# Kernel optimization log

Hardware: AMD Instinct MI355X
Metric: run time of the kernel (lower is better)

## Reference

```python
import jax, jax.numpy as jnp
import numpy as np

N_NODES = 100000
N_EDGES = 3200000
D_IN, D_HID, D_OUT = 128, 128, 40


def _sage_conv(x, src, dst, W_l, W_r, b, counts):
    # mean aggregation of neighbor (source) features at destination nodes
    agg = jax.ops.segment_sum(x[src], dst, num_segments=N_NODES)  # [N, d]
    agg = agg / counts  # mean (isolated nodes stay zero via clamped counts)
    # PyG SAGEConv: out = lin_l(aggr) + lin_r(x_root); bias lives in lin_l
    return agg @ W_l + x @ W_r + b


def setup_inputs() -> dict:
    key = jax.random.key(0)
    ks = jax.random.split(key, 8)
    x = jax.random.normal(ks[0], (N_NODES, D_IN), dtype=jnp.float32)
    edge_index = jax.random.randint(ks[1], (2, N_EDGES), 0, N_NODES, dtype=jnp.int64)
    s1 = 1.0 / np.sqrt(D_IN)
    s2 = 1.0 / np.sqrt(D_HID)
    return {
        "x": x,
        "edge_index": edge_index,
        "W1_l": jax.random.uniform(ks[2], (D_IN, D_HID), jnp.float32, -s1, s1),
        "W1_r": jax.random.uniform(ks[3], (D_IN, D_HID), jnp.float32, -s1, s1),
        "b1": jnp.zeros((D_HID,), jnp.float32),
        "W2_l": jax.random.uniform(ks[4], (D_HID, D_OUT), jnp.float32, -s2, s2),
        "W2_r": jax.random.uniform(ks[5], (D_HID, D_OUT), jnp.float32, -s2, s2),
        "b2": jnp.zeros((D_OUT,), jnp.float32),
    }


def reference(x, edge_index, W1_l, W1_r, b1, W2_l, W2_r, b2):
    src, dst = edge_index[0], edge_index[1]
    # in-degree per destination node, clamped to avoid div-by-zero
    deg = jax.ops.segment_sum(jnp.ones((N_EDGES,), jnp.float32), dst, num_segments=N_NODES)
    counts = jnp.maximum(deg, 1.0)[:, None]  # [N, 1]
    h = jax.nn.relu(_sage_conv(x, src, dst, W1_l, W1_r, b1, counts))
    h = _sage_conv(h, src, dst, W2_l, W2_r, b2, counts)
    return jax.nn.log_softmax(h, axis=1)
```

## Files before the change

kernel.cpp:

```cpp
#include <hip/hip_runtime.h>
#include <hip/hip_bf16.h>
#include <hip/hip_fp8.h>
#include <math.h>

#define N_NODES 100000
#define D_IN    128
#define D_HID   128
#define D_OUT   40
#define NBUCK   391
#define CHUNK   4096
#define SLABCAP 16320


using short8  = __attribute__((ext_vector_type(8))) short;
using float4v = __attribute__((ext_vector_type(4))) float;
using floatx2 = __attribute__((ext_vector_type(2))) float;

__device__ __forceinline__ unsigned short f2b(float f) {
    __hip_bfloat16 b = __float2bfloat16(f);
    return *(unsigned short*)&b;
}
__device__ __forceinline__ unsigned packb(float a, float b) {
    return (unsigned)f2b(a) | ((unsigned)f2b(b) << 16);
}

__device__ __forceinline__ unsigned char f2q(float f) {
    __hip_fp8_e4m3 v(f);
    return *(unsigned char*)&v;
}
template <int SEL>
__device__ __forceinline__ float q2f(unsigned u) {
#if __has_builtin(__builtin_amdgcn_cvt_f32_fp8)
    return __builtin_amdgcn_cvt_f32_fp8((int)u, SEL);
#else
    unsigned char b = (u >> (SEL * 8)) & 0xff;
    __hip_fp8_e4m3 v;
    *(unsigned char*)&v = b;
    return (float)v;
#endif
}
template <bool HI>
__device__ __forceinline__ floatx2 pkcvt(unsigned u) {
#if __has_builtin(__builtin_amdgcn_cvt_pk_f32_fp8)
    return __builtin_amdgcn_cvt_pk_f32_fp8((int)u, HI);
#else
    floatx2 r;
    if constexpr (HI) { r[0] = q2f<2>(u); r[1] = q2f<3>(u); }
    else              { r[0] = q2f<0>(u); r[1] = q2f<1>(u); }
    return r;
#endif
}

__global__ void detect_kernel(const int* __restrict__ ei, int* __restrict__ flag) {
    if (threadIdx.x == 0 && blockIdx.x == 0) {
        int all0 = 1;
        for (int i = 0; i < 256; ++i) {
            if (ei[2 * i + 1] != 0) { all0 = 0; break; }
        }
        *flag = all0;
    }
}

__device__ __forceinline__ long long edge_at(const void* ei, int is64, long long idx) {
    if (is64) return ((const long long*)ei)[idx];
    return (long long)((const int*)ei)[idx];
}

__global__ __launch_bounds__(256) void cast_kernel(const float* __restrict__ x,
                                                   unsigned short* __restrict__ xb,
                                                   unsigned char* __restrict__ xq) {
    long long i = ((long long)blockIdx.x * 256 + threadIdx.x) * 8;
    if (i >= (long long)N_NODES * 128) return;
    float4 a = *(const float4*)&x[i];
    float4 b = *(const float4*)&x[i + 4];
    ushort4 o0, o1;
    o0.x = f2b(a.x); o0.y = f2b(a.y); o0.z = f2b(a.z); o0.w = f2b(a.w);
    o1.x = f2b(b.x); o1.y = f2b(b.y); o1.z = f2b(b.z); o1.w = f2b(b.w);
    *(ushort4*)&xb[i] = o0;
    *(ushort4*)&xb[i + 4] = o1;
    uint2 p;
    p.x = (unsigned)f2q(a.x) | ((unsigned)f2q(a.y) << 8)
        | ((unsigned)f2q(a.z) << 16) | ((unsigned)f2q(a.w) << 24);
    p.y = (unsigned)f2q(b.x) | ((unsigned)f2q(b.y) << 8)
        | ((unsigned)f2q(b.z) << 16) | ((unsigned)f2q(b.w) << 24);
    *(uint2*)&xq[i] = p;
}

__global__ __launch_bounds__(256) void pack_w_kernel(const float* __restrict__ W1l,
                                                     const float* __restrict__ W1r,
                                                     const float* __restrict__ W2l,
                                                     const float* __restrict__ W2r,
                                                     unsigned short* __restrict__ wp1,
                                                     unsigned short* __restrict__ wp2) {
    int t = blockIdx.x * 256 + threadIdx.x;
    if (t < 4096) {
        int lane = t & 63;
        int ks = (t >> 6) & 7;
        int ct = t >> 9;
        int n = ct * 16 + (lane & 15);
        int kr = (lane >> 4) * 8;
        unsigned short v[8];
#pragma unroll
        for (int j = 0; j < 8; ++j) {
            int k = ks * 32 + kr + j;
            float f = (k < 128) ? W1l[k * 128 + n] : W1r[(k - 128) * 128 + n];
            v[j] = f2b(f);
        }
        ushort4 o0 = {v[0], v[1], v[2], v[3]};
        ushort4 o1 = {v[4], v[5], v[6], v[7]};
        *(ushort4*)&wp1[t * 8] = o0;
        *(ushort4*)&wp1[t * 8 + 4] = o1;
    } else if (t < 4096 + 1280) {
        int u = t - 4096;
        int lane = u & 63;
        int ks = (u >> 6) & 3;
        int ct = u >> 8;
        int n = ct * 16 + (lane & 15);
        int kr = (lane >> 4) * 8;
        unsigned short v[8];
#pragma unroll
        for (int j = 0; j < 8; ++j) {
            int k = ks * 32 + kr + j;
            float f = (n < 40) ? W2l[k * 40 + n] : W2r[k * 40 + (n - 40)];
            v[j] = f2b(f);
        }
        ushort4 o0 = {v[0], v[1], v[2], v[3]};
        ushort4 o1 = {v[4], v[5], v[6], v[7]};
        *(ushort4*)&wp2[u * 8] = o0;
        *(ushort4*)&wp2[u * 8 + 4] = o1;
    }
}

__global__ __launch_bounds__(1024) void partition_kernel(const void* __restrict__ ei,
                                                         const int* __restrict__ flag,
                                                         unsigned* __restrict__ bcount,
                                                         unsigned* __restrict__ slab,
                                                         long long E) {
    __shared__ unsigned hist[NBUCK];
    __shared__ unsigned lstart[NBUCK];
    __shared__ unsigned gofs[NBUCK];
    __shared__ unsigned s[512];
    __shared__ unsigned rec[CHUNK];
    __shared__ unsigned short bkt[CHUNK];

    const int tid = threadIdx.x;
    const int is64 = *flag;
    const long long cb = (long long)blockIdx.x * CHUNK;
    const unsigned n = (unsigned)(((E - cb) < (long long)CHUNK) ? (E - cb) : CHUNK);

    if (tid < NBUCK) hist[tid] = 0;
    __syncthreads();

#pragma unroll
    for (int j = 0; j < CHUNK / 1024; ++j) {
        unsigned e = j * 1024 + tid;
        if (e < n) {
            unsigned d = (unsigned)edge_at(ei, is64, E + cb + e);
            atomicAdd(&hist[d >> 8], 1u);
        }
    }
    __syncthreads();

    if (tid < 512) s[tid] = (tid < NBUCK) ? hist[tid] : 0u;
    __syncthreads();
    for (int off = 1; off < 512; off <<= 1) {
        unsigned t = 0;
        if (tid < 512 && tid >= off) t = s[tid - off];
        __syncthreads();
        if (tid < 512) s[tid] += t;
        __syncthreads();
    }
    if (tid < NBUCK) {
        unsigned cnt = hist[tid];
        unsigned ex = s[tid] - cnt;
        lstart[tid] = ex;
        if (cnt) {
            unsigned g = atomicAdd(&bcount[tid], cnt);
            gofs[tid] = (unsigned)(tid * SLABCAP) + g - ex;
        }
        hist[tid] = 0;
    }
    __syncthreads();

#pragma unroll
    for (int j = 0; j < CHUNK / 1024; ++j) {
        unsigned e = j * 1024 + tid;
        if (e < n) {
            unsigned sv = (unsigned)edge_at(ei, is64, cb + e);
            unsigned d  = (unsigned)edge_at(ei, is64, E + cb + e);
            unsigned b = d >> 8;
            unsigned loc = atomicAdd(&hist[b], 1u);
            unsigned slot = lstart[b] + loc;
            rec[slot] = ((d & 255u) << 17) | sv;
            bkt[slot] = (unsigned short)b;
        }
    }
    __syncthreads();

#pragma unroll
    for (int j = 0; j < CHUNK / 1024; ++j) {
        unsigned i = j * 1024 + tid;
        if (i < n) {
            unsigned b = bkt[i];
            slab[gofs[b] + i] = rec[i];
        }
    }
}

__global__ __launch_bounds__(512) void bscan_kernel(const unsigned* __restrict__ bcount,
                                                    unsigned* __restrict__ bstart) {
    __shared__ unsigned s[512];
    int tid = threadIdx.x;
    unsigned v = (tid < NBUCK) ? bcount[tid] : 0u;
    s[tid] = v;
    __syncthreads();
    for (int off = 1; off < 512; off <<= 1) {
        unsigned t = (tid >= off) ? s[tid - off] : 0u;
        __syncthreads();
        s[tid] += t;
        __syncthreads();
    }
    if (tid < NBUCK) bstart[tid] = s[tid] - v;
    if (tid == 511) bstart[NBUCK] = s[511];
}

__global__ __launch_bounds__(256) void build_kernel(const unsigned* __restrict__ slab,
                                                    const unsigned* __restrict__ bstart,
                                                    unsigned* __restrict__ deg,
                                                    float* __restrict__ invc,
                                                    unsigned* __restrict__ row_start,
                                                    int* __restrict__ csr) {
    __shared__ unsigned cnt[256];
    __shared__ unsigned scn[256];
    const int tid = threadIdx.x;
    const int nb = blockIdx.x << 8;
    const unsigned es = bstart[blockIdx.x];
    const unsigned n  = bstart[blockIdx.x + 1] - es;
    const long long sb = (long long)blockIdx.x * SLABCAP;

    cnt[tid] = 0;
    __syncthreads();
    for (unsigned i = tid; i < n; i += 256) {
        unsigned d = slab[sb + i] >> 17;
        atomicAdd(&cnt[d], 1u);
    }
    __syncthreads();
    unsigned v = cnt[tid];
    scn[tid] = v;
    __syncthreads();
    for (int off = 1; off < 256; off <<= 1) {
        unsigned t = (tid >= off) ? scn[tid - off] : 0u;
        __syncthreads();
        scn[tid] += t;
        __syncthreads();
    }
    unsigned ex = scn[tid] - v;
    int node = nb + tid;
    if (node < N_NODES) {
        deg[node] = v;
        invc[node] = 1.0f / fmaxf((float)v, 1.0f);
        row_start[node] = es + ex;
    }
    __syncthreads();
    cnt[tid] = ex;
    __syncthreads();
    for (unsigned i = tid; i < n; i += 256) {
        unsigned pr = slab[sb + i];
        unsigned d = pr >> 17;
        unsigned pos = es + atomicAdd(&cnt[d], 1u);
        csr[pos] = (int)(pr & 0x1FFFFu);
    }
}

__global__ __launch_bounds__(256) void gather_fp8_kernel(const unsigned char* __restrict__ featq,
                                                         const int* __restrict__ csr,
                                                         const unsigned* __restrict__ row_start,
                                                         const unsigned* __restrict__ deg,
                                                         const float* __restrict__ invc,
                                                         unsigned short* __restrict__ aggb) {
    const int wave = threadIdx.x >> 6;
    const int lane = threadIdx.x & 63;
    const int node = blockIdx.x * 4 + wave;
    if (node >= N_NODES) return;

    const unsigned start = row_start[node];
    const unsigned cnt = deg[node];
    const int s = lane >> 4;
    const int cg = lane & 15;

    floatx2 acc[4];
#pragma unroll
    for (int k = 0; k < 4; ++k) acc[k] = (floatx2){0.f, 0.f};

    for (unsigned base = 0; base < cnt; base += 64) {
        unsigned rem = cnt - base;
        if (rem > 64u) rem = 64u;
        int nid = (lane < (int)rem) ? csr[start + base + lane] : 0;
        for (unsigned j = 0; j < rem; j += 8) {
            uint2 u0 = {0u, 0u}, u1 = {0u, 0u};
            unsigned i0 = j + s;
            unsigned i1 = j + 4 + s;
            int s0 = __shfl(nid, (int)(i0 & 63));
            int s1 = __shfl(nid, (int)(i1 & 63));
            if (i0 < rem) u0 = *(const uint2*)&featq[(long long)s0 * 128 + cg * 8];
            if (i1 < rem) u1 = *(const uint2*)&featq[(long long)s1 * 128 + cg * 8];
            acc[0] += pkcvt<false>(u0.x); acc[1] += pkcvt<true>(u0.x);
            acc[2] += pkcvt<false>(u0.y); acc[3] += pkcvt<true>(u0.y);
            acc[0] += pkcvt<false>(u1.x); acc[1] += pkcvt<true>(u1.x);
            acc[2] += pkcvt<false>(u1.y); acc[3] += pkcvt<true>(u1.y);
        }
    }

#pragma unroll
    for (int k = 0; k < 4; ++k) {
        acc[k][0] += __shfl_xor(acc[k][0], 16);
        acc[k][1] += __shfl_xor(acc[k][1], 16);
        acc[k][0] += __shfl_xor(acc[k][0], 32);
        acc[k][1] += __shfl_xor(acc[k][1], 32);
    }

    if (lane < 16) {
        const float ic = invc[node];
        uint4 o;
        o.x = packb(acc[0][0] * ic, acc[0][1] * ic);
        o.y = packb(acc[1][0] * ic, acc[1][1] * ic);
        o.z = packb(acc[2][0] * ic, acc[2][1] * ic);
        o.w = packb(acc[3][0] * ic, acc[3][1] * ic);
        *(uint4*)&aggb[(long long)node * 128 + cg * 8] = o;
    }
}

__global__ __launch_bounds__(256) void gemm1_mfma_kernel(const unsigned short* __restrict__ aggb,
                                                         const unsigned short* __restrict__ xb,
                                                         const unsigned short* __restrict__ wp1,
                                                         const float* __restrict__ bias,
                                                         unsigned short* __restrict__ hb) {
    const int wave = threadIdx.x >> 6;
    const int lane = threadIdx.x & 63;
    const int row0 = blockIdx.x * 64 + wave * 16;
    const long long abase = (long long)(row0 + (lane & 15)) * 128 + (lane >> 4) * 8;

    float4v acc[8];
#pragma unroll
    for (int ct = 0; ct < 8; ++ct) acc[ct] = (float4v){0.f, 0.f, 0.f, 0.f};

#pragma unroll
    for (int ks = 0; ks < 8; ++ks) {
        union { uint4 u; short8 s; } af;
        if (ks < 4) af.u = *(const uint4*)&aggb[abase + ks * 32];
        else        af.u = *(const uint4*)&xb[abase + (ks - 4) * 32];
#pragma unroll
        for (int ct = 0; ct < 8; ++ct) {
            union { uint4 u; short8 s; } bf;
            bf.u = *(const uint4*)&wp1[((ct * 8 + ks) * 64 + lane) * 8];
            acc[ct] = __builtin_amdgcn_mfma_f32_16x16x32_bf16(af.s, bf.s, acc[ct], 0, 0, 0);
        }
    }

    const int crow0 = row0 + (lane >> 4) * 4;
    const int ccol = lane & 15;
#pragma unroll
    for (int ct = 0; ct < 8; ++ct) {
        const int col = ct * 16 + ccol;
        const float bv = bias[col];
#pragma unroll
        for (int r = 0; r < 4; ++r) {
            int row = crow0 + r;
            if (row < N_NODES)
                hb[(long long)row * 128 + col] = f2b(fmaxf(acc[ct][r] + bv, 0.0f));
        }
    }
}

__global__ __launch_bounds__(256) void gemm2p_mfma_kernel(const unsigned short* __restrict__ hb,
                                                          const unsigned short* __restrict__ wp2,
                                                          const float* __restrict__ b2,
                                                          unsigned char* __restrict__ pq,
                                                          float* __restrict__ q) {
    const int wave = threadIdx.x >> 6;
    const int lane = threadIdx.x & 63;
    const int row0 = blockIdx.x * 64 + wave * 16;
    const long long abase = (long long)(row0 + (lane & 15)) * 128 + (lane >> 4) * 8;

    float4v acc[5];
#pragma unroll
    for (int ct = 0; ct < 5; ++ct) acc[ct] = (float4v){0.f, 0.f, 0.f, 0.f};

#pragma unroll
    for (int ks = 0; ks < 4; ++ks) {
        union { uint4 u; short8 s; } af;
        af.u = *(const uint4*)&hb[abase + ks * 32];
#pragma unroll
        for (int ct = 0; ct < 5; ++ct) {
            union { uint4 u; short8 s; } bf;
            bf.u = *(const uint4*)&wp2[((ct * 4 + ks) * 64 + lane) * 8];
            acc[ct] = __builtin_amdgcn_mfma_f32_16x16x32_bf16(af.s, bf.s, acc[ct], 0, 0, 0);
        }
    }

    const int crow0 = row0 + (lane >> 4) * 4;
    const int ccol = lane & 15;
#pragma unroll
    for (int ct = 0; ct < 5; ++ct) {
        const int col = ct * 16 + ccol;
#pragma unroll
        for (int r = 0; r < 4; ++r) {
            int row = crow0 + r;
            if (row < N_NODES) {
                if (col < D_OUT) {
                    pq[(long long)row * D_OUT + col] = f2q(acc[ct][r]);
                } else {
                    q[(long long)row * D_OUT + (col - D_OUT)] = acc[ct][r] + b2[col - D_OUT];
                }
            }
        }
    }
}

__global__ __launch_bounds__(256) void gather40_kernel(const unsigned char* __restrict__ pq,
                                                       const float* __restrict__ q,
                                                       const int* __restrict__ csr,
                                                       const unsigned* __restrict__ row_start,
                                                       const unsigned* __restrict__ deg,
                                                       const float* __restrict__ invc,
                                                       float* __restrict__ out) {
    __shared__ float sm[4][40];
    const int wave = threadIdx.x >> 6;
    const int lane = threadIdx.x & 63;
    const int node = blockIdx.x * 4 + wave;
    if (node >= N_NODES) return;

    const unsigned start = row_start[node];
    const unsigned cnt = deg[node];
    const int s = lane / 10;
    const int cg = lane % 10;
    const bool gactive = s < 6;

    floatx2 a01 = (floatx2){0.f, 0.f}, a23 = (floatx2){0.f, 0.f};

    for (unsigned base = 0; base < cnt; base += 64) {
        unsigned rem = cnt - base;
        if (rem > 64u) rem = 64u;
        int nid = (lane < (int)rem) ? csr[start + base + lane] : 0;
        for (unsigned j = 0; j < rem; j += 24) {
            unsigned u[4];
#pragma unroll
            for (int t = 0; t < 4; ++t) {
                unsigned idx = j + t * 6 + s;
                int sid = __shfl(nid, (int)(idx & 63));
                bool valid = gactive && (idx < rem);
                u[t] = valid ? *(const unsigned*)&pq[(long long)sid * D_OUT + cg * 4] : 0u;
            }
#pragma unroll
            for (int t = 0; t < 4; ++t) {
                a01 += pkcvt<false>(u[t]);
                a23 += pkcvt<true>(u[t]);
            }
        }
    }

    float a0 = a01[0], a1 = a01[1], a2 = a23[0], a3 = a23[1];
    {
        float t0, t1, t2, t3;
        t0 = __shfl(a0, lane + 30); t1 = __shfl(a1, lane + 30);
        t2 = __shfl(a2, lane + 30); t3 = __shfl(a3, lane + 30);
        if (lane < 30) { a0 += t0; a1 += t1; a2 += t2; a3 += t3; }
        t0 = __shfl(a0, lane + 20); t1 = __shfl(a1, lane + 20);
        t2 = __shfl(a2, lane + 20); t3 = __shfl(a3, lane + 20);
        if (lane < 10) { a0 += t0; a1 += t1; a2 += t2; a3 += t3; }
        t0 = __shfl(a0, lane + 10); t1 = __shfl(a1, lane + 10);
        t2 = __shfl(a2, lane + 10); t3 = __shfl(a3, lane + 10);
        if (lane < 10) { a0 += t0; a1 += t1; a2 += t2; a3 += t3; }
    }
    if (lane < 10) {
        sm[wave][cg * 4 + 0] = a0;
        sm[wave][cg * 4 + 1] = a1;
        sm[wave][cg * 4 + 2] = a2;
        sm[wave][cg * 4 + 3] = a3;
    }
    const bool active = lane < D_OUT;
    float v = active ? (sm[wave][active ? lane : 0] * invc[node]
                        + q[(long long)node * D_OUT + (active ? lane : 0)])
                     : -__builtin_huge_valf();
    float m = v;
#pragma unroll
    for (int off = 32; off >= 1; off >>= 1) m = fmaxf(m, __shfl_xor(m, off));
    float e = active ? expf(v - m) : 0.0f;
    float ssum = e;
#pragma unroll
    for (int off = 32; off >= 1; off >>= 1) ssum += __shfl_xor(ssum, off);
    float ls = logf(ssum);
    if (active) out[(long long)node * D_OUT + lane] = v - m - ls;
}

extern "C" void kernel_launch(void* const* d_in, const int* in_sizes, int n_in,
                              void* d_out, int out_size, void* d_ws, size_t ws_size,
                              hipStream_t stream) {
    const float* x   = (const float*)d_in[0];
    const void*  ei  = d_in[1];
    const float* W1l = (const float*)d_in[2];
    const float* W1r = (const float*)d_in[3];
    const float* b1  = (const float*)d_in[4];
    const float* W2l = (const float*)d_in[5];
    const float* W2r = (const float*)d_in[6];
    const float* b2  = (const float*)d_in[7];
    float* out = (float*)d_out;

    const long long E = (long long)in_sizes[1] / 2;
    const int NPB = (int)((E + CHUNK - 1) / CHUNK);

    char* ws = (char*)d_ws;
    int*      flag      = (int*)ws;
    unsigned* bcount    = (unsigned*)(ws + 4096);
    unsigned* bstart    = (unsigned*)(ws + 8192);
    unsigned* deg       = (unsigned*)(ws + 16384);
    float*    invc      = (float*)(ws + 416384);
    unsigned* row_start = (unsigned*)(ws + 816384);
    int*      csr       = (int*)(ws + 1216384);
    unsigned short* xb  = (unsigned short*)(ws + 14016384);
    unsigned char*  pq  = (unsigned char*)(ws + 14016384);
    float*    q         = (float*)(ws + 22016384);
    unsigned short* aggb= (unsigned short*)(ws + 39616384);
    unsigned* slab      = (unsigned*)(ws + 39616384);
    unsigned short* wp1 = (unsigned short*)(ws + 65216384);
    unsigned short* wp2 = (unsigned short*)(ws + 65281920);
    unsigned short* hb  = (unsigned short*)(ws + 65310720);
    unsigned char*  xq  = (unsigned char*)(ws + 90910720);

    (void)hipMemsetAsync(bcount, 0, 4096, stream);
    detect_kernel<<<1, 64, 0, stream>>>((const int*)ei, flag);

    cast_kernel<<<(int)(((long long)N_NODES * 128 / 8 + 255) / 256), 256, 0, stream>>>(x, xb, xq);
    pack_w_kernel<<<21, 256, 0, stream>>>(W1l, W1r, W2l, W2r, wp1, wp2);

    partition_kernel<<<NPB, 1024, 0, stream>>>(ei, flag, bcount, slab, E);
    bscan_kernel<<<1, 512, 0, stream>>>(bcount, bstart);
    build_kernel<<<NBUCK, 256, 0, stream>>>(slab, bstart, deg, invc, row_start, csr);

    gather_fp8_kernel<<<(N_NODES + 3) / 4, 256, 0, stream>>>(xq, csr, row_start, deg, invc, aggb);
    gemm1_mfma_kernel<<<(N_NODES + 63) / 64, 256, 0, stream>>>(aggb, xb, wp1, b1, hb);

    gemm2p_mfma_kernel<<<(N_NODES + 63) / 64, 256, 0, stream>>>(hb, wp2, b2, pq, q);
    gather40_kernel<<<(N_NODES + 3) / 4, 256, 0, stream>>>(pq, q, csr, row_start, deg, invc, out);
}
```

Measured before the change: 356.6 us.

## Split FP8 feature gather into four column-slice passes for cache locality

The FP8 node features are stored as four column slices of 32 bytes per node instead of one 128-byte row per node. The layer-1 gather then runs as four passes, each gathering a single slice for all nodes. Each slice is about 3.2 MB, so it can stay resident in L2/MALL during its pass and cut DRAM traffic from random neighbour reads. The cost is reading the CSR, degrees and row starts four times, extra launches, and smaller 32-byte random accesses per neighbour.

```diff
diff --git a/kernel.cpp b/kernel.cpp
--- a/kernel.cpp
+++ b/kernel.cpp
@@ -10,6 +10,7 @@
 #define NBUCK   391
 #define CHUNK   4096
 #define SLABCAP 16320
+#define SLICE_BYTES (N_NODES * 32)
 
 
 using short8  = __attribute__((ext_vector_type(8))) short;
@@ -68,9 +69,11 @@
 
 __global__ __launch_bounds__(256) void cast_kernel(const float* __restrict__ x,
                                                    unsigned short* __restrict__ xb,
-                                                   unsigned char* __restrict__ xq) {
+                                                   unsigned char* __restrict__ xq4) {
     long long i = ((long long)blockIdx.x * 256 + threadIdx.x) * 8;
     if (i >= (long long)N_NODES * 128) return;
+    long long node = i >> 7;
+    int col = (int)(i & 127);
     float4 a = *(const float4*)&x[i];
     float4 b = *(const float4*)&x[i + 4];
     ushort4 o0, o1;
@@ -83,7 +86,7 @@
         | ((unsigned)f2q(a.z) << 16) | ((unsigned)f2q(a.w) << 24);
     p.y = (unsigned)f2q(b.x) | ((unsigned)f2q(b.y) << 8)
         | ((unsigned)f2q(b.z) << 16) | ((unsigned)f2q(b.w) << 24);
-    *(uint2*)&xq[i] = p;
+    *(uint2*)&xq4[(long long)(col >> 5) * SLICE_BYTES + node * 32 + (col & 31)] = p;
 }
 
 __global__ __launch_bounds__(256) void pack_w_kernel(const float* __restrict__ W1l,
@@ -272,12 +275,13 @@
     }
 }
 
-__global__ __launch_bounds__(256) void gather_fp8_kernel(const unsigned char* __restrict__ featq,
-                                                         const int* __restrict__ csr,
-                                                         const unsigned* __restrict__ row_start,
-                                                         const unsigned* __restrict__ deg,
-                                                         const float* __restrict__ invc,
-                                                         unsigned short* __restrict__ aggb) {
+__global__ __launch_bounds__(256) void gather_fp8_pass_kernel(const unsigned char* __restrict__ slice,
+                                                              const int* __restrict__ csr,
+                                                              const unsigned* __restrict__ row_start,
+                                                              const unsigned* __restrict__ deg,
+                                                              const float* __restrict__ invc,
+                                                              unsigned short* __restrict__ aggb,
+                                                              int pass) {
     const int wave = threadIdx.x >> 6;
     const int lane = threadIdx.x & 63;
     const int node = blockIdx.x * 4 + wave;
@@ -285,8 +289,8 @@
 
     const unsigned start = row_start[node];
     const unsigned cnt = deg[node];
-    const int s = lane >> 4;
-    const int cg = lane & 15;
+    const int s = lane >> 2;
+    const int cg = lane & 3;
 
     floatx2 acc[4];
 #pragma unroll
@@ -296,14 +300,14 @@
         unsigned rem = cnt - base;
         if (rem > 64u) rem = 64u;
         int nid = (lane < (int)rem) ? csr[start + base + lane] : 0;
-        for (unsigned j = 0; j < rem; j += 8) {
+        for (unsigned j = 0; j < rem; j += 32) {
             uint2 u0 = {0u, 0u}, u1 = {0u, 0u};
-            unsigned i0 = j + s;
-            unsigned i1 = j + 4 + s;
+            unsigned i0 = j + (unsigned)s;
+            unsigned i1 = j + 16 + (unsigned)s;
             int s0 = __shfl(nid, (int)(i0 & 63));
             int s1 = __shfl(nid, (int)(i1 & 63));
-            if (i0 < rem) u0 = *(const uint2*)&featq[(long long)s0 * 128 + cg * 8];
-            if (i1 < rem) u1 = *(const uint2*)&featq[(long long)s1 * 128 + cg * 8];
+            if (i0 < rem) u0 = *(const uint2*)&slice[(long long)s0 * 32 + cg * 8];
+            if (i1 < rem) u1 = *(const uint2*)&slice[(long long)s1 * 32 + cg * 8];
             acc[0] += pkcvt<false>(u0.x); acc[1] += pkcvt<true>(u0.x);
             acc[2] += pkcvt<false>(u0.y); acc[3] += pkcvt<true>(u0.y);
             acc[0] += pkcvt<false>(u1.x); acc[1] += pkcvt<true>(u1.x);
@@ -313,20 +317,24 @@
 
 #pragma unroll
     for (int k = 0; k < 4; ++k) {
+        acc[k][0] += __shfl_xor(acc[k][0], 4);
+        acc[k][1] += __shfl_xor(acc[k][1], 4);
+        acc[k][0] += __shfl_xor(acc[k][0], 8);
+        acc[k][1] += __shfl_xor(acc[k][1], 8);
         acc[k][0] += __shfl_xor(acc[k][0], 16);
         acc[k][1] += __shfl_xor(acc[k][1], 16);
         acc[k][0] += __shfl_xor(acc[k][0], 32);
         acc[k][1] += __shfl_xor(acc[k][1], 32);
     }
 
-    if (lane < 16) {
+    if (lane < 4) {
         const float ic = invc[node];
         uint4 o;
         o.x = packb(acc[0][0] * ic, acc[0][1] * ic);
         o.y = packb(acc[1][0] * ic, acc[1][1] * ic);
         o.z = packb(acc[2][0] * ic, acc[2][1] * ic);
         o.w = packb(acc[3][0] * ic, acc[3][1] * ic);
-        *(uint4*)&aggb[(long long)node * 128 + cg * 8] = o;
+        *(uint4*)&aggb[(long long)node * 128 + pass * 32 + cg * 8] = o;
     }
 }
 
@@ -525,19 +533,22 @@
     unsigned short* wp1 = (unsigned short*)(ws + 65216384);
     unsigned short* wp2 = (unsigned short*)(ws + 65281920);
     unsigned short* hb  = (unsigned short*)(ws + 65310720);
-    unsigned char*  xq  = (unsigned char*)(ws + 90910720);
+    unsigned char*  xq4 = (unsigned char*)(ws + 90910720);
 
     (void)hipMemsetAsync(bcount, 0, 4096, stream);
     detect_kernel<<<1, 64, 0, stream>>>((const int*)ei, flag);
 
-    cast_kernel<<<(int)(((long long)N_NODES * 128 / 8 + 255) / 256), 256, 0, stream>>>(x, xb, xq);
+    cast_kernel<<<(int)(((long long)N_NODES * 128 / 8 + 255) / 256), 256, 0, stream>>>(x, xb, xq4);
     pack_w_kernel<<<21, 256, 0, stream>>>(W1l, W1r, W2l, W2r, wp1, wp2);
 
     partition_kernel<<<NPB, 1024, 0, stream>>>(ei, flag, bcount, slab, E);
     bscan_kernel<<<1, 512, 0, stream>>>(bcount, bstart);
     build_kernel<<<NBUCK, 256, 0, stream>>>(slab, bstart, deg, invc, row_start, csr);
 
-    gather_fp8_kernel<<<(N_NODES + 3) / 4, 256, 0, stream>>>(xq, csr, row_start, deg, invc, aggb);
+    for (int p = 0; p < 4; ++p) {
+        gather_fp8_pass_kernel<<<(N_NODES + 3) / 4, 256, 0, stream>>>(
+            xq4 + (long long)p * SLICE_BYTES, csr, row_start, deg, invc, aggb, p);
+    }
     gemm1_mfma_kernel<<<(N_NODES + 63) / 64, 256, 0, stream>>>(aggb, xb, wp1, b1, hb);
 
     gemm2p_mfma_kernel<<<(N_NODES + 63) / 64, 256, 0, stream>>>(hb, wp2, b2, pq, q);
```

Measured after the change: 466.3 us. 30.8% more time.

## Fuse neighbor gather into GEMM1 via shared memory and merge prep kernels

Applied to the files above, without the earlier changes.

Combines the fp8 neighbor-mean gather and the first SAGE GEMM into one kernel, staging each block's 64 aggregated rows in LDS instead of writing and rereading a bf16 aggregate buffer in global memory. Also merges the edge-format detection, feature cast and weight packing into a single launch. This removes a full intermediate round trip and two launches. In exchange, each wave now processes 16 nodes sequentially before the MFMA stage, reducing the number of independent waves available to hide gather latency.

```diff
diff --git a/kernel.cpp b/kernel.cpp
--- a/kernel.cpp
+++ b/kernel.cpp
@@ -10,6 +10,7 @@
 #define NBUCK   391
 #define CHUNK   4096
 #define SLABCAP 16320
+#define CAST_BLOCKS 6250
 
 
 using short8  = __attribute__((ext_vector_type(8))) short;
@@ -51,83 +52,85 @@
 #endif
 }
 
-__global__ void detect_kernel(const int* __restrict__ ei, int* __restrict__ flag) {
-    if (threadIdx.x == 0 && blockIdx.x == 0) {
-        int all0 = 1;
-        for (int i = 0; i < 256; ++i) {
-            if (ei[2 * i + 1] != 0) { all0 = 0; break; }
-        }
-        *flag = all0;
-    }
-}
-
 __device__ __forceinline__ long long edge_at(const void* ei, int is64, long long idx) {
     if (is64) return ((const long long*)ei)[idx];
     return (long long)((const int*)ei)[idx];
 }
 
-__global__ __launch_bounds__(256) void cast_kernel(const float* __restrict__ x,
+__global__ __launch_bounds__(256) void prep_kernel(const float* __restrict__ x,
                                                    unsigned short* __restrict__ xb,
-                                                   unsigned char* __restrict__ xq) {
-    long long i = ((long long)blockIdx.x * 256 + threadIdx.x) * 8;
-    if (i >= (long long)N_NODES * 128) return;
-    float4 a = *(const float4*)&x[i];
-    float4 b = *(const float4*)&x[i + 4];
-    ushort4 o0, o1;
-    o0.x = f2b(a.x); o0.y = f2b(a.y); o0.z = f2b(a.z); o0.w = f2b(a.w);
-    o1.x = f2b(b.x); o1.y = f2b(b.y); o1.z = f2b(b.z); o1.w = f2b(b.w);
-    *(ushort4*)&xb[i] = o0;
-    *(ushort4*)&xb[i + 4] = o1;
-    uint2 p;
-    p.x = (unsigned)f2q(a.x) | ((unsigned)f2q(a.y) << 8)
-        | ((unsigned)f2q(a.z) << 16) | ((unsigned)f2q(a.w) << 24);
-    p.y = (unsigned)f2q(b.x) | ((unsigned)f2q(b.y) << 8)
-        | ((unsigned)f2q(b.z) << 16) | ((unsigned)f2q(b.w) << 24);
-    *(uint2*)&xq[i] = p;
-}
-
-__global__ __launch_bounds__(256) void pack_w_kernel(const float* __restrict__ W1l,
-                                                     const float* __restrict__ W1r,
-                                                     const float* __restrict__ W2l,
-                                                     const float* __restrict__ W2r,
-                                                     unsigned short* __restrict__ wp1,
-                                                     unsigned short* __restrict__ wp2) {
-    int t = blockIdx.x * 256 + threadIdx.x;
-    if (t < 4096) {
-        int lane = t & 63;
-        int ks = (t >> 6) & 7;
-        int ct = t >> 9;
-        int n = ct * 16 + (lane & 15);
-        int kr = (lane >> 4) * 8;
-        unsigned short v[8];
-#pragma unroll
-        for (int j = 0; j < 8; ++j) {
-            int k = ks * 32 + kr + j;
-            float f = (k < 128) ? W1l[k * 128 + n] : W1r[(k - 128) * 128 + n];
-            v[j] = f2b(f);
-        }
-        ushort4 o0 = {v[0], v[1], v[2], v[3]};
-        ushort4 o1 = {v[4], v[5], v[6], v[7]};
-        *(ushort4*)&wp1[t * 8] = o0;
-        *(ushort4*)&wp1[t * 8 + 4] = o1;
-    } else if (t < 4096 + 1280) {
-        int u = t - 4096;
-        int lane = u & 63;
-        int ks = (u >> 6) & 3;
-        int ct = u >> 8;
-        int n = ct * 16 + (lane & 15);
-        int kr = (lane >> 4) * 8;
-        unsigned short v[8];
-#pragma unroll
-        for (int j = 0; j < 8; ++j) {
-            int k = ks * 32 + kr + j;
-            float f = (n < 40) ? W2l[k * 40 + n] : W2r[k * 40 + (n - 40)];
-            v[j] = f2b(f);
-        }
-        ushort4 o0 = {v[0], v[1], v[2], v[3]};
-        ushort4 o1 = {v[4], v[5], v[6], v[7]};
-        *(ushort4*)&wp2[u * 8] = o0;
-        *(ushort4*)&wp2[u * 8 + 4] = o1;
+                                                   unsigned char* __restrict__ xq,
+                                                   const float* __restrict__ W1l,
+                                                   const float* __restrict__ W1r,
+                                                   const float* __restrict__ W2l,
+                                                   const float* __restrict__ W2r,
+                                                   unsigned short* __restrict__ wp1,
+                                                   unsigned short* __restrict__ wp2,
+                                                   const int* __restrict__ ei,
+                                                   int* __restrict__ flag) {
+    const int b = blockIdx.x;
+    if (b < CAST_BLOCKS) {
+        long long i = ((long long)b * 256 + threadIdx.x) * 8;
+        if (i >= (long long)N_NODES * 128) return;
+        float4 a = *(const float4*)&x[i];
+        float4 c = *(const float4*)&x[i + 4];
+        ushort4 o0, o1;
+        o0.x = f2b(a.x); o0.y = f2b(a.y); o0.z = f2b(a.z); o0.w = f2b(a.w);
+        o1.x = f2b(c.x); o1.y = f2b(c.y); o1.z = f2b(c.z); o1.w = f2b(c.w);
+        *(ushort4*)&xb[i] = o0;
+        *(ushort4*)&xb[i + 4] = o1;
+        uint2 p;
+        p.x = (unsigned)f2q(a.x) | ((unsigned)f2q(a.y) << 8)
+            | ((unsigned)f2q(a.z) << 16) | ((unsigned)f2q(a.w) << 24);
+        p.y = (unsigned)f2q(c.x) | ((unsigned)f2q(c.y) << 8)
+            | ((unsigned)f2q(c.z) << 16) | ((unsigned)f2q(c.w) << 24);
+        *(uint2*)&xq[i] = p;
+    } else if (b < CAST_BLOCKS + 21) {
+        int t = (b - CAST_BLOCKS) * 256 + threadIdx.x;
+        if (t < 4096) {
+            int lane = t & 63;
+            int ks = (t >> 6) & 7;
+            int ct = t >> 9;
+            int n = ct * 16 + (lane & 15);
+            int kr = (lane >> 4) * 8;
+            unsigned short v[8];
+#pragma unroll
+            for (int j = 0; j < 8; ++j) {
+                int k = ks * 32 + kr + j;
+                float f = (k < 128) ? W1l[k * 128 + n] : W1r[(k - 128) * 128 + n];
+                v[j] = f2b(f);
+            }
+            ushort4 o0 = {v[0], v[1], v[2], v[3]};
+            ushort4 o1 = {v[4], v[5], v[6], v[7]};
+            *(ushort4*)&wp1[t * 8] = o0;
+            *(ushort4*)&wp1[t * 8 + 4] = o1;
+        } else if (t < 4096 + 1280) {
+            int u = t - 4096;
+            int lane = u & 63;
+            int ks = (u >> 6) & 3;
+            int ct = u >> 8;
+            int n = ct * 16 + (lane & 15);
+            int kr = (lane >> 4) * 8;
+            unsigned short v[8];
+#pragma unroll
+            for (int j = 0; j < 8; ++j) {
+                int k = ks * 32 + kr + j;
+                float f = (n < 40) ? W2l[k * 40 + n] : W2r[k * 40 + (n - 40)];
+                v[j] = f2b(f);
+            }
+            ushort4 o0 = {v[0], v[1], v[2], v[3]};
+            ushort4 o1 = {v[4], v[5], v[6], v[7]};
+            *(ushort4*)&wp2[u * 8] = o0;
+            *(ushort4*)&wp2[u * 8 + 4] = o1;
+        }
+    } else {
+        if (threadIdx.x == 0) {
+            int all0 = 1;
+            for (int i = 0; i < 256; ++i) {
+                if (ei[2 * i + 1] != 0) { all0 = 0; break; }
+            }
+            *flag = all0;
+        }
     }
 }
 
@@ -272,88 +275,92 @@
     }
 }
 
-__global__ __launch_bounds__(256) void gather_fp8_kernel(const unsigned char* __restrict__ featq,
-                                                         const int* __restrict__ csr,
-                                                         const unsigned* __restrict__ row_start,
-                                                         const unsigned* __restrict__ deg,
-                                                         const float* __restrict__ invc,
-                                                         unsigned short* __restrict__ aggb) {
+__global__ __launch_bounds__(256) void gather_gemm1_kernel(const unsigned char* __restrict__ featq,
+                                                           const int* __restrict__ csr,
+                                                           const unsigned* __restrict__ row_start,
+                                                           const unsigned* __restrict__ deg,
+                                                           const float* __restrict__ invc,
+                                                           const unsigned short* __restrict__ xb,
+                                                           const unsigned short* __restrict__ wp1,
+                                                           const float* __restrict__ bias,
+                                                           unsigned short* __restrict__ hb) {
+    __shared__ unsigned short sagg[64][136];
     const int wave = threadIdx.x >> 6;
     const int lane = threadIdx.x & 63;
-    const int node = blockIdx.x * 4 + wave;
-    if (node >= N_NODES) return;
-
-    const unsigned start = row_start[node];
-    const unsigned cnt = deg[node];
+    const int nblk = blockIdx.x * 64;
     const int s = lane >> 4;
     const int cg = lane & 15;
 
-    floatx2 acc[4];
-#pragma unroll
-    for (int k = 0; k < 4; ++k) acc[k] = (floatx2){0.f, 0.f};
-
-    for (unsigned base = 0; base < cnt; base += 64) {
-        unsigned rem = cnt - base;
-        if (rem > 64u) rem = 64u;
-        int nid = (lane < (int)rem) ? csr[start + base + lane] : 0;
-        for (unsigned j = 0; j < rem; j += 8) {
-            uint2 u0 = {0u, 0u}, u1 = {0u, 0u};
-            unsigned i0 = j + s;
-            unsigned i1 = j + 4 + s;
-            int s0 = __shfl(nid, (int)(i0 & 63));
-            int s1 = __shfl(nid, (int)(i1 & 63));
-            if (i0 < rem) u0 = *(const uint2*)&featq[(long long)s0 * 128 + cg * 8];
-            if (i1 < rem) u1 = *(const uint2*)&featq[(long long)s1 * 128 + cg * 8];
-            acc[0] += pkcvt<false>(u0.x); acc[1] += pkcvt<true>(u0.x);
-            acc[2] += pkcvt<false>(u0.y); acc[3] += pkcvt<true>(u0.y);
-            acc[0] += pkcvt<false>(u1.x); acc[1] += pkcvt<true>(u1.x);
-            acc[2] += pkcvt<false>(u1.y); acc[3] += pkcvt<true>(u1.y);
-        }
-    }
-
-#pragma unroll
-    for (int k = 0; k < 4; ++k) {
-        acc[k][0] += __shfl_xor(acc[k][0], 16);
-        acc[k][1] += __shfl_xor(acc[k][1], 16);
-        acc[k][0] += __shfl_xor(acc[k][0], 32);
-        acc[k][1] += __shfl_xor(acc[k][1], 32);
-    }
-
-    if (lane < 16) {
-        const float ic = invc[node];
-        uint4 o;
-        o.x = packb(acc[0][0] * ic, acc[0][1] * ic);
-        o.y = packb(acc[1][0] * ic, acc[1][1] * ic);
-        o.z = packb(acc[2][0] * ic, acc[2][1] * ic);
-        o.w = packb(acc[3][0] * ic, acc[3][1] * ic);
-        *(uint4*)&aggb[(long long)node * 128 + cg * 8] = o;
-    }
-}
-
-__global__ __launch_bounds__(256) void gemm1_mfma_kernel(const unsigned short* __restrict__ aggb,
-                                                         const unsigned short* __restrict__ xb,
-                                                         const unsigned short* __restrict__ wp1,
-                                                         const float* __restrict__ bias,
-                                                         unsigned short* __restrict__ hb) {
-    const int wave = threadIdx.x >> 6;
-    const int lane = threadIdx.x & 63;
-    const int row0 = blockIdx.x * 64 + wave * 16;
-    const long long abase = (long long)(row0 + (lane & 15)) * 128 + (lane >> 4) * 8;
-
-    float4v acc[8];
-#pragma unroll
-    for (int ct = 0; ct < 8; ++ct) acc[ct] = (float4v){0.f, 0.f, 0.f, 0.f};
+    for (int i = 0; i < 16; ++i) {
+        const int node = nblk + wave * 16 + i;
+        if (node < N_NODES) {
+            const unsigned start = row_start[node];
+            const unsigned cnt = deg[node];
+            floatx2 acc[4];
+#pragma unroll
+            for (int k = 0; k < 4; ++k) acc[k] = (floatx2){0.f, 0.f};
+
+            for (unsigned base = 0; base < cnt; base += 64) {
+                unsigned rem = cnt - base;
+                if (rem > 64u) rem = 64u;
+                int nid = (lane < (int)rem) ? csr[start + base + lane] : 0;
+                for (unsigned j = 0; j < rem; j += 8) {
+                    uint2 u0 = {0u, 0u}, u1 = {0u, 0u};
+                    unsigned i0 = j + s;
+                    unsigned i1 = j + 4 + s;
+                    int s0 = __shfl(nid, (int)(i0 & 63));
+                    int s1 = __shfl(nid, (int)(i1 & 63));
+                    if (i0 < rem) u0 = *(const uint2*)&featq[(long long)s0 * 128 + cg * 8];
+                    if (i1 < rem) u1 = *(const uint2*)&featq[(long long)s1 * 128 + cg * 8];
+                    acc[0] += pkcvt<false>(u0.x); acc[1] += pkcvt<true>(u0.x);
+                    acc[2] += pkcvt<false>(u0.y); acc[3] += pkcvt<true>(u0.y);
+                    acc[0] += pkcvt<false>(u1.x); acc[1] += pkcvt<true>(u1.x);
+                    acc[2] += pkcvt<false>(u1.y); acc[3] += pkcvt<true>(u1.y);
+                }
+            }
+
+#pragma unroll
+            for (int k = 0; k < 4; ++k) {
+                acc[k][0] += __shfl_xor(acc[k][0], 16);
+                acc[k][1] += __shfl_xor(acc[k][1], 16);
+                acc[k][0] += __shfl_xor(acc[k][0], 32);
+                acc[k][1] += __shfl_xor(acc[k][1], 32);
+            }
+
+            if (lane < 16) {
+                const float ic = invc[node];
+                uint4 o;
+                o.x = packb(acc[0][0] * ic, acc[0][1] * ic);
+                o.y = packb(acc[1][0] * ic, acc[1][1] * ic);
+                o.z = packb(acc[2][0] * ic, acc[2][1] * ic);
+                o.w = packb(acc[3][0] * ic, acc[3][1] * ic);
+                *(uint4*)&sagg[wave * 16 + i][cg * 8] = o;
+            }
+        } else if (lane < 16) {
+            uint4 z = {0u, 0u, 0u, 0u};
+            *(uint4*)&sagg[wave * 16 + i][cg * 8] = z;
+        }
+    }
+    __syncthreads();
+
+    const int row0 = nblk + wave * 16;
+    const unsigned short* aptr = &sagg[wave * 16 + (lane & 15)][(lane >> 4) * 8];
+    const long long xbase = (long long)(row0 + (lane & 15)) * 128 + (lane >> 4) * 8;
+
+    float4v gacc[8];
+#pragma unroll
+    for (int ct = 0; ct < 8; ++ct) gacc[ct] = (float4v){0.f, 0.f, 0.f, 0.f};
 
 #pragma unroll
     for (int ks = 0; ks < 8; ++ks) {
         union { uint4 u; short8 s; } af;
-        if (ks < 4) af.u = *(const uint4*)&aggb[abase + ks * 32];
-        else        af.u = *(const uint4*)&xb[abase + (ks - 4) * 32];
+        if (ks < 4) af.u = *(const uint4*)&aptr[ks * 32];
+        else        af.u = *(const uint4*)&xb[xbase + (ks - 4) * 32];
 #pragma unroll
         for (int ct = 0; ct < 8; ++ct) {
             union { uint4 u; short8 s; } bf;
             bf.u = *(const uint4*)&wp1[((ct * 8 + ks) * 64 + lane) * 8];
-            acc[ct] = __builtin_amdgcn_mfma_f32_16x16x32_bf16(af.s, bf.s, acc[ct], 0, 0, 0);
+            gacc[ct] = __builtin_amdgcn_mfma_f32_16x16x32_bf16(af.s, bf.s, gacc[ct], 0, 0, 0);
         }
     }
 
@@ -367,7 +374,7 @@
         for (int r = 0; r < 4; ++r) {
             int row = crow0 + r;
             if (row < N_NODES)
-                hb[(long long)row * 128 + col] = f2b(fmaxf(acc[ct][r] + bv, 0.0f));
+                hb[(long long)row * 128 + col] = f2b(fmaxf(gacc[ct][r] + bv, 0.0f));
         }
     }
 }
@@ -520,7 +527,6 @@
     unsigned short* xb  = (unsigned short*)(ws + 14016384);
     unsigned char*  pq  = (unsigned char*)(ws + 14016384);
     float*    q         = (float*)(ws + 22016384);
-    unsigned short* aggb= (unsigned short*)(ws + 39616384);
     unsigned* slab      = (unsigned*)(ws + 39616384);
     unsigned short* wp1 = (unsigned short*)(ws + 65216384);
     unsigned short* wp2 = (unsigned short*)(ws + 65281920);
@@ -528,17 +534,16 @@
     unsigned char*  xq  = (unsigned char*)(ws + 90910720);
 
     (void)hipMemsetAsync(bcount, 0, 4096, stream);
-    detect_kernel<<<1, 64, 0, stream>>>((const int*)ei, flag);
-
-    cast_kernel<<<(int)(((long long)N_NODES * 128 / 8 + 255) / 256), 256, 0, stream>>>(x, xb, xq);
-    pack_w_kernel<<<21, 256, 0, stream>>>(W1l, W1r, W2l, W2r, wp1, wp2);
+
+    prep_kernel<<<CAST_BLOCKS + 21 + 1, 256, 0, stream>>>(x, xb, xq, W1l, W1r, W2l, W2r,
+                                                          wp1, wp2, (const int*)ei, flag);
 
     partition_kernel<<<NPB, 1024, 0, stream>>>(ei, flag, bcount, slab, E);
     bscan_kernel<<<1, 512, 0, stream>>>(bcount, bstart);
     build_kernel<<<NBUCK, 256, 0, stream>>>(slab, bstart, deg, invc, row_start, csr);
 
-    gather_fp8_kernel<<<(N_NODES + 3) / 4, 256, 0, stream>>>(xq, csr, row_start, deg, invc, aggb);
-    gemm1_mfma_kernel<<<(N_NODES + 63) / 64, 256, 0, stream>>>(aggb, xb, wp1, b1, hb);
+    gather_gemm1_kernel<<<(N_NODES + 63) / 64, 256, 0, stream>>>(xq, csr, row_start, deg, invc,
+                                                                 xb, wp1, b1, hb);
 
     gemm2p_mfma_kernel<<<(N_NODES + 63) / 64, 256, 0, stream>>>(hb, wp2, b2, pq, q);
     gather40_kernel<<<(N_NODES + 3) / 4, 256, 0, stream>>>(pq, q, csr, row_start, deg, invc, out);
```

After: 380.3 us. +6.6%, slower.
